# Kernel optimization log

Hardware: AMD Instinct MI355X
Metric: run time of the kernel (lower is better)

Reference implementation:

```python
import jax, jax.numpy as jnp
import numpy as np

CUTOFF = 1.0  # nm
KE = 138.96   # Coulomb constant conversion factor used by the module


def physnet_attenuation(r, cutoff=CUTOFF):
    # PhysNet smooth switching function: 1 - 6u^5 + 15u^4 - 10u^3 for u<1, else 0
    u = r / cutoff
    phi = 1.0 - 6.0 * u**5 + 15.0 * u**4 - 10.0 * u**3
    return jnp.where(u < 1.0, phi, 0.0)


def setup_inputs() -> dict:
    key = jax.random.key(0)
    k1, k2, k3, k4 = jax.random.split(key, 4)
    N = 262144          # total atoms
    P = 16777216        # total pairs (~64 neighbors/atom)
    S = 1024            # number of systems
    pair_idx = jax.random.randint(k1, (2, P), 0, N, dtype=jnp.int32)
    # distances in (0.05, 1.25) nm; 2*d straddles the cutoff so both branches of chi_r are exercised
    d_ij = (jax.random.uniform(k2, (P, 1), dtype=jnp.float32) * 1.2 + 0.05)
    charge = jax.random.normal(k3, (N, 1), dtype=jnp.float32) * 0.3
    sys_idx = jnp.sort(jax.random.randint(k4, (N,), 0, S, dtype=jnp.int32))
    return {
        "electrostatic_pair_indices": pair_idx,
        "electrostatic_d_ij": d_ij,
        "per_atom_charge": charge,
        "atomic_subsystem_indices": sys_idx,
        "num_systems": S,
    }


def reference(electrostatic_pair_indices, electrostatic_d_ij, per_atom_charge,
              atomic_subsystem_indices, num_systems):
    idx_i = electrostatic_pair_indices[0]
    idx_j = electrostatic_pair_indices[1]
    # unique-pair mask (static shapes: zero out instead of filtering)
    mask = idx_i < idx_j
    d = electrostatic_d_ij[:, 0]                       # [P]
    q = per_atom_charge[:, 0]                          # [N]
    phi_2r = physnet_attenuation(2.0 * d)
    chi_r = phi_2r / jnp.sqrt(d * d + 1.0) + (1.0 - phi_2r) / d
    e_pair = q[idx_i] * q[idx_j] * chi_r               # [P]
    e_pair = jnp.where(mask, e_pair, 0.0)
    seg = atomic_subsystem_indices[idx_i]              # system of each pair
    per_system = jax.ops.segment_sum(e_pair, seg, num_segments=num_systems)
    return (per_system * KE)[:, None]                  # [S, 1]
```

## Files before the change

### kernel.cpp

```cpp
#include <hip/hip_runtime.h>

typedef int   v4i __attribute__((ext_vector_type(4)));
typedef float v4f __attribute__((ext_vector_type(4)));

#define S_SYS    1024
#define KE_CONST 138.96f
#define BLOCKS   1024
#define THREADS  512
#define NWAVE    (THREADS / 64)

__global__ __launch_bounds__(256) void pack_kernel(const float* __restrict__ q,
                                                   const int* __restrict__ sys,
                                                   float2* __restrict__ packed, int N) {
    int i = blockIdx.x * blockDim.x + threadIdx.x;
    if (i < N) {
        float2 v;
        v.x = q[i];
        v.y = __int_as_float(sys[i]);
        packed[i] = v;
    }
}

__global__ __launch_bounds__(THREADS, 8) void pair_kernel(const v4i* __restrict__ idx_i4,
                                                          const v4i* __restrict__ idx_j4,
                                                          const v4f* __restrict__ d4,
                                                          const float2* __restrict__ packed,
                                                          float* __restrict__ partial,
                                                          int P4) {
    __shared__ float acc[NWAVE][S_SYS];
    const int tid = threadIdx.x;
    const int wave = tid >> 6;
    for (int t = tid; t < NWAVE * S_SYS; t += THREADS) ((float*)acc)[t] = 0.0f;
    __syncthreads();

    const int stride = gridDim.x * blockDim.x;
    for (int p = blockIdx.x * blockDim.x + tid; p < P4; p += 2 * stride) {
        const int p2 = p + stride;
        const bool has2 = (p2 < P4);

        v4i vi0 = __builtin_nontemporal_load(&idx_i4[p]);
        v4i vj0 = __builtin_nontemporal_load(&idx_j4[p]);
        v4f vd0 = __builtin_nontemporal_load(&d4[p]);
        v4i vi1 = {0, 0, 0, 0};
        v4i vj1 = {0, 0, 0, 0};
        v4f vd1 = {1.f, 1.f, 1.f, 1.f};
        if (has2) {
            vi1 = __builtin_nontemporal_load(&idx_i4[p2]);
            vj1 = __builtin_nontemporal_load(&idx_j4[p2]);
            vd1 = __builtin_nontemporal_load(&d4[p2]);
        }

        int   ii[8], jj[8];
        float dd[8];
#pragma unroll
        for (int k = 0; k < 4; ++k) { ii[k] = vi0[k];     jj[k] = vj0[k];     dd[k] = vd0[k]; }
#pragma unroll
        for (int k = 0; k < 4; ++k) { ii[4 + k] = vi1[k]; jj[4 + k] = vj1[k]; dd[4 + k] = vd1[k]; }

        float2 pi[8];
        float  qj[8];
#pragma unroll
        for (int k = 0; k < 8; ++k) {
            if (ii[k] < jj[k]) {
                pi[k] = packed[ii[k]];
                qj[k] = packed[jj[k]].x;
            }
        }

#pragma unroll
        for (int k = 0; k < 8; ++k) {
            if (ii[k] < jj[k]) {
                float d   = dd[k];
                float u   = 2.0f * d;
                float phi = 0.0f;
                if (u < 1.0f) {
                    float u3 = u * u * u;
                    phi = 1.0f - u3 * (10.0f + u * (6.0f * u - 15.0f));
                }
                float rcp = __builtin_amdgcn_rcpf(d);
                float chi = rcp + phi * (__builtin_amdgcn_rsqf(d * d + 1.0f) - rcp);
                float e   = pi[k].x * qj[k] * chi;
                atomicAdd(&acc[wave][__float_as_int(pi[k].y)], e);
            }
        }
    }
    __syncthreads();
    for (int s = tid; s < S_SYS; s += THREADS) {
        float v = 0.0f;
#pragma unroll
        for (int w = 0; w < NWAVE; ++w) v += acc[w][s];
        partial[(size_t)blockIdx.x * S_SYS + s] = v;
    }
}

__global__ __launch_bounds__(256) void reduce_kernel(const float* __restrict__ partial,
                                                     float* __restrict__ out, int B) {
    int s = blockIdx.x;
    float sum = 0.0f;
    for (int b = threadIdx.x; b < B; b += blockDim.x)
        sum += partial[(size_t)b * S_SYS + s];
#pragma unroll
    for (int off = 32; off > 0; off >>= 1) sum += __shfl_down(sum, off, 64);
    __shared__ float wsum[4];
    if ((threadIdx.x & 63) == 0) wsum[threadIdx.x >> 6] = sum;
    __syncthreads();
    if (threadIdx.x == 0) out[s] = KE_CONST * (wsum[0] + wsum[1] + wsum[2] + wsum[3]);
}

extern "C" void kernel_launch(void* const* d_in, const int* in_sizes, int n_in,
                              void* d_out, int out_size, void* d_ws, size_t ws_size,
                              hipStream_t stream) {
    const int*   pair = (const int*)d_in[0];
    const float* d_ij = (const float*)d_in[1];
    const float* q    = (const float*)d_in[2];
    const int*   sys  = (const int*)d_in[3];
    const int P = in_sizes[1];
    const int N = in_sizes[2];
    float* out = (float*)d_out;

    float2* packed  = (float2*)d_ws;
    float*  partial = (float*)((char*)d_ws + (size_t)N * sizeof(float2));

    pack_kernel<<<(N + 255) / 256, 256, 0, stream>>>(q, sys, packed, N);

    pair_kernel<<<BLOCKS, THREADS, 0, stream>>>(
        (const v4i*)pair, (const v4i*)(pair + P), (const v4f*)d_ij,
        packed, partial, P / 4);

    reduce_kernel<<<S_SYS, 256, 0, stream>>>(partial, out, BLOCKS);
}
```

Baseline: 300.0 us.

## Drop reduce kernel via global atomics and make pair loop branch-free

Removes the separate reduce kernel and partial buffer: each block now atomically adds its scaled per-system sums straight into the output, which the pack kernel zeroes first. The pair loop no longer branches on the i<j mask. Gathers use index 0 for masked pairs, and masked lanes add zero to a per-lane dummy bin, so every lane runs the same instructions and the LDS atomics are spread out. Launch bounds are relaxed from 8 to 4 blocks per CU. The trade-off is about a million global float atomics in a nondeterministic order, plus extra LDS atomics and gathers for masked pairs, in exchange for less divergence and one fewer launch.

```diff
diff --git a/kernel.cpp b/kernel.cpp
--- a/kernel.cpp
+++ b/kernel.cpp
@@ -11,7 +11,8 @@
 
 __global__ __launch_bounds__(256) void pack_kernel(const float* __restrict__ q,
                                                    const int* __restrict__ sys,
-                                                   float2* __restrict__ packed, int N) {
+                                                   float2* __restrict__ packed,
+                                                   float* __restrict__ out, int N) {
     int i = blockIdx.x * blockDim.x + threadIdx.x;
     if (i < N) {
         float2 v;
@@ -19,17 +20,19 @@
         v.y = __int_as_float(sys[i]);
         packed[i] = v;
     }
+    if (i < S_SYS) out[i] = 0.0f;
 }
 
-__global__ __launch_bounds__(THREADS, 8) void pair_kernel(const v4i* __restrict__ idx_i4,
+__global__ __launch_bounds__(THREADS, 4) void pair_kernel(const v4i* __restrict__ idx_i4,
                                                           const v4i* __restrict__ idx_j4,
                                                           const v4f* __restrict__ d4,
                                                           const float2* __restrict__ packed,
-                                                          float* __restrict__ partial,
+                                                          float* __restrict__ out,
                                                           int P4) {
     __shared__ float acc[NWAVE][S_SYS];
-    const int tid = threadIdx.x;
+    const int tid  = threadIdx.x;
     const int wave = tid >> 6;
+    const int lane = tid & 63;
     for (int t = tid; t < NWAVE * S_SYS; t += THREADS) ((float*)acc)[t] = 0.0f;
     __syncthreads();
 
@@ -57,54 +60,47 @@
 #pragma unroll
         for (int k = 0; k < 4; ++k) { ii[4 + k] = vi1[k]; jj[4 + k] = vj1[k]; dd[4 + k] = vd1[k]; }
 
+        bool act[8];
+        int  gi[8], gj[8];
+#pragma unroll
+        for (int k = 0; k < 8; ++k) {
+            act[k] = ii[k] < jj[k];
+            gi[k]  = act[k] ? ii[k] : 0;
+            gj[k]  = act[k] ? jj[k] : 0;
+        }
         float2 pi[8];
         float  qj[8];
 #pragma unroll
         for (int k = 0; k < 8; ++k) {
-            if (ii[k] < jj[k]) {
-                pi[k] = packed[ii[k]];
-                qj[k] = packed[jj[k]].x;
-            }
+            pi[k] = packed[gi[k]];
+            qj[k] = packed[gj[k]].x;
         }
 
 #pragma unroll
         for (int k = 0; k < 8; ++k) {
-            if (ii[k] < jj[k]) {
-                float d   = dd[k];
-                float u   = 2.0f * d;
-                float phi = 0.0f;
-                if (u < 1.0f) {
-                    float u3 = u * u * u;
-                    phi = 1.0f - u3 * (10.0f + u * (6.0f * u - 15.0f));
-                }
-                float rcp = __builtin_amdgcn_rcpf(d);
-                float chi = rcp + phi * (__builtin_amdgcn_rsqf(d * d + 1.0f) - rcp);
-                float e   = pi[k].x * qj[k] * chi;
-                atomicAdd(&acc[wave][__float_as_int(pi[k].y)], e);
+            float d   = dd[k];
+            float u   = 2.0f * d;
+            float phi = 0.0f;
+            if (u < 1.0f) {
+                float u3 = u * u * u;
+                phi = 1.0f - u3 * (10.0f + u * (6.0f * u - 15.0f));
             }
+            float rcp = __builtin_amdgcn_rcpf(d);
+            float chi = rcp + phi * (__builtin_amdgcn_rsqf(d * d + 1.0f) - rcp);
+            float e   = pi[k].x * qj[k] * chi;
+            float es  = act[k] ? e : 0.0f;
+            int   bin = act[k] ? __float_as_int(pi[k].y) : lane;
+            atomicAdd(&acc[wave][bin], es);
         }
     }
     __syncthreads();
+
     for (int s = tid; s < S_SYS; s += THREADS) {
         float v = 0.0f;
 #pragma unroll
         for (int w = 0; w < NWAVE; ++w) v += acc[w][s];
-        partial[(size_t)blockIdx.x * S_SYS + s] = v;
+        atomicAdd(&out[s], KE_CONST * v);
     }
-}
-
-__global__ __launch_bounds__(256) void reduce_kernel(const float* __restrict__ partial,
-                                                     float* __restrict__ out, int B) {
-    int s = blockIdx.x;
-    float sum = 0.0f;
-    for (int b = threadIdx.x; b < B; b += blockDim.x)
-        sum += partial[(size_t)b * S_SYS + s];
-#pragma unroll
-    for (int off = 32; off > 0; off >>= 1) sum += __shfl_down(sum, off, 64);
-    __shared__ float wsum[4];
-    if ((threadIdx.x & 63) == 0) wsum[threadIdx.x >> 6] = sum;
-    __syncthreads();
-    if (threadIdx.x == 0) out[s] = KE_CONST * (wsum[0] + wsum[1] + wsum[2] + wsum[3]);
 }
 
 extern "C" void kernel_launch(void* const* d_in, const int* in_sizes, int n_in,
@@ -118,14 +114,11 @@
     const int N = in_sizes[2];
     float* out = (float*)d_out;
 
-    float2* packed  = (float2*)d_ws;
-    float*  partial = (float*)((char*)d_ws + (size_t)N * sizeof(float2));
+    float2* packed = (float2*)d_ws;
 
-    pack_kernel<<<(N + 255) / 256, 256, 0, stream>>>(q, sys, packed, N);
+    pack_kernel<<<(N + 255) / 256, 256, 0, stream>>>(q, sys, packed, out, N);
 
     pair_kernel<<<BLOCKS, THREADS, 0, stream>>>(
         (const v4i*)pair, (const v4i*)(pair + P), (const v4f*)d_ij,
-        packed, partial, P / 4);
-
-    reduce_kernel<<<S_SYS, 256, 0, stream>>>(partial, out, BLOCKS);
+        packed, out, P / 4);
 }
```

Measured after the change: 296.5 us. Within noise of the previous version (-1.2%).
